# Performance work log

Hardware: AMD Instinct MI355X
Metric: run time of the kernel (lower is better)

The kernel has to match this reference:

```python
import jax, jax.numpy as jnp
import numpy as np


def setup_inputs() -> dict:
    key = jax.random.key(0)
    ks = jax.random.split(key, 5)
    S, B, H = 4096, 32, 512
    scale = 1.0 / np.sqrt(2 * H)
    return {
        "hidden": jax.random.normal(ks[0], (B, H), dtype=jnp.float32),
        "encoder_outputs": jax.random.normal(ks[1], (S, B, H), dtype=jnp.float32),
        "attn_W": jax.random.normal(ks[2], (H, 2 * H), dtype=jnp.float32) * scale,
        "attn_b": jax.random.normal(ks[3], (H,), dtype=jnp.float32) * scale,
        "v_W": jax.random.normal(ks[4], (1, H), dtype=jnp.float32) * (1.0 / np.sqrt(H)),
    }


def reference(hidden, encoder_outputs, attn_W, attn_b, v_W):
    # hidden: [B,H], encoder_outputs: [S,B,H]
    # energy = tanh(concat(hidden_rep, enc) @ attn_W.T + attn_b)
    # Split attn_W into the hidden-part and encoder-part to avoid
    # materializing the repeated/concatenated [S,B,2H] tensor.
    H = hidden.shape[-1]
    Wh, We = attn_W[:, :H], attn_W[:, H:]  # each [H, H]
    # hidden contribution is identical for all seq positions: [B,H]
    h_proj = jnp.einsum('bh,oh->bo', hidden, Wh) + attn_b
    e_proj = jnp.einsum('sbh,oh->sbo', encoder_outputs, We)
    energy = jnp.tanh(h_proj[None, :, :] + e_proj)          # [S,B,H]
    scores = jnp.einsum('sbh,h->sb', energy, v_W[0])        # [S,B]
    attn_weights = jax.nn.softmax(scores.T, axis=1)         # [B,S]
    # context = sum_s w[b,s] * enc[s,b,:]
    context = jnp.einsum('bs,sbh->bh', attn_weights, encoder_outputs)
    return (context, attn_weights)
```

## Files before the change

### kernel.cpp

```cpp
#include <hip/hip_runtime.h>
#include <hip/hip_bf16.h>
#include <math.h>

#define S 4096
#define B 32
#define H 512
#define NSC 16

typedef float f32x16 __attribute__((ext_vector_type(16)));
typedef short s16x8 __attribute__((ext_vector_type(8)));

__device__ __forceinline__ unsigned short f2bf(float x) {
  return __builtin_bit_cast(unsigned short, __float2bfloat16(x));
}
__device__ __forceinline__ float bf2f(unsigned short h) {
  return __builtin_bit_cast(float, ((unsigned)h) << 16);
}
__device__ __forceinline__ float tanh_fast(float x) {
  float e = __expf(2.0f * x);
  return 1.0f - 2.0f / (e + 1.0f);
}

#define GLOAD_LDS16(g, l) __builtin_amdgcn_global_load_lds( \
    (const __attribute__((address_space(1))) void*)(g),     \
    (__attribute__((address_space(3))) void*)(l), 16, 0, 0)

__global__ __launch_bounds__(256) void k_wfrag(const float* __restrict__ W,
                                               unsigned short* __restrict__ WH,
                                               unsigned short* __restrict__ WL) {
  int id = blockIdx.x * 256 + threadIdx.x;
  int lane = id & 63, ks = (id >> 6) & 31, n = id >> 11;
  int o = n * 32 + (lane & 31);
  int kb = ks * 16 + (lane >> 5) * 8;
  const float* src = W + (size_t)o * (2 * H) + H + kb;
  s16x8 h, l;
#pragma unroll
  for (int j = 0; j < 8; ++j) {
    float x = src[j];
    unsigned short hb = f2bf(x);
    h[j] = (short)hb;
    l[j] = (short)f2bf(x - bf2f(hb));
  }
  *(s16x8*)(WH + (size_t)id * 8) = h;
  *(s16x8*)(WL + (size_t)id * 8) = l;
}

__global__ __launch_bounds__(256) void k_hproj(const float* __restrict__ hidden,
                                               const float* __restrict__ W,
                                               const float* __restrict__ bias,
                                               float* __restrict__ hprojT) {
  int blk = blockIdx.x;
  int b = blk >> 3, oc = blk & 7;
  int t = threadIdx.x;
  int o = oc * 64 + (t >> 2);
  int kq = t & 3;
  const float* hrow = hidden + b * H + kq * 128;
  const float* wrow = W + (size_t)o * (2 * H) + kq * 128;
  float p = 0.f;
#pragma unroll 4
  for (int k = 0; k < 128; ++k) p = fmaf(hrow[k], wrow[k], p);
  p += __shfl_xor(p, 1);
  p += __shfl_xor(p, 2);
  if (kq == 0) hprojT[o * B + b] = p + bias[o];
}

#define MFMA32(a, b, c) __builtin_amdgcn_mfma_f32_32x32x16_bf16(a, b, c, 0, 0, 0)

#define STAGE(dstbuf, ph)                                          \
  {                                                                \
    const char* gh_ = WHb + (size_t)(ph) * 16384;                  \
    const char* gl_ = WLb + (size_t)(ph) * 16384;                  \
    _Pragma("unroll")                                              \
    for (int i_ = 0; i_ < 4; ++i_) {                               \
      int co_ = (w * 4 + i_) * 1024;                               \
      GLOAD_LDS16(gh_ + co_ + lane * 16, dstbuf + co_);            \
      GLOAD_LDS16(gl_ + co_ + lane * 16, dstbuf + 16384 + co_);    \
    }                                                              \
  }

__global__ __launch_bounds__(256, 1) void k_scores(const float* __restrict__ enc,
                                                   const char* __restrict__ WHb,
                                                   const char* __restrict__ WLb,
                                                   const float* __restrict__ hprojT,
                                                   const float* __restrict__ vW,
                                                   float* __restrict__ scores) {
  __shared__ char Bb0[32768];
  __shared__ char Bb1[32768];
  int t = threadIdx.x;
  int w = t >> 6, lane = t & 63;
  int wbase = blockIdx.x * 128 + w * 32;
  int arow = wbase + (lane & 31);
  int half = lane >> 5;

  STAGE(Bb0, 0);

  s16x8 ah[32], al[32];
  {
    const float* ap = enc + (size_t)arow * H + half * 8;
#pragma unroll
    for (int ks = 0; ks < 32; ++ks) {
      float4 x0 = *(const float4*)(ap + ks * 16);
      float4 x1 = *(const float4*)(ap + ks * 16 + 4);
      float xs[8] = {x0.x, x0.y, x0.z, x0.w, x1.x, x1.y, x1.z, x1.w};
      s16x8 h, l;
#pragma unroll
      for (int j = 0; j < 8; ++j) {
        unsigned short hb = f2bf(xs[j]);
        h[j] = (short)hb;
        l[j] = (short)f2bf(xs[j] - bf2f(hb));
      }
      ah[ks] = h;
      al[ks] = l;
    }
  }

  float pr[16];
#pragma unroll
  for (int r = 0; r < 16; ++r) pr[r] = 0.f;

  __syncthreads();

  for (int n = 0; n < 16; ++n) {
    f32x16 chh = {}, chl = {}, clh = {};
    STAGE(Bb1, 2 * n + 1);
#pragma unroll
    for (int ks = 0; ks < 16; ++ks) {
      s16x8 b0 = *(const s16x8*)(Bb0 + ks * 1024 + lane * 16);
      s16x8 b1 = *(const s16x8*)(Bb0 + 16384 + ks * 1024 + lane * 16);
      chh = MFMA32(ah[ks], b0, chh);
      chl = MFMA32(ah[ks], b1, chl);
      clh = MFMA32(al[ks], b0, clh);
    }
    __syncthreads();
    if (n < 15) STAGE(Bb0, 2 * n + 2);
#pragma unroll
    for (int ks = 0; ks < 16; ++ks) {
      s16x8 b0 = *(const s16x8*)(Bb1 + ks * 1024 + lane * 16);
      s16x8 b1 = *(const s16x8*)(Bb1 + 16384 + ks * 1024 + lane * 16);
      chh = MFMA32(ah[16 + ks], b0, chh);
      chl = MFMA32(ah[16 + ks], b1, chl);
      clh = MFMA32(al[16 + ks], b0, clh);
    }
    {
      int o = n * 32 + (lane & 31);
      float vw = vW[o];
      const float4* hp4 = (const float4*)(hprojT + o * B + half * 4);
      float4 h0 = hp4[0], h1 = hp4[2], h2 = hp4[4], h3 = hp4[6];
      float hr[16] = {h0.x, h0.y, h0.z, h0.w, h1.x, h1.y, h1.z, h1.w,
                      h2.x, h2.y, h2.z, h2.w, h3.x, h3.y, h3.z, h3.w};
#pragma unroll
      for (int r = 0; r < 16; ++r) {
        float e = (chh[r] + chl[r]) + clh[r] + hr[r];
        pr[r] += vw * tanh_fast(e);
      }
    }
    __syncthreads();
  }

#pragma unroll
  for (int off = 1; off < 32; off <<= 1) {
#pragma unroll
    for (int r = 0; r < 16; ++r) pr[r] += __shfl_xor(pr[r], off);
  }
  if ((lane & 31) == 0) {
    int srow = wbase >> 5;
#pragma unroll
    for (int r = 0; r < 16; ++r) {
      int m = (r & 3) + 8 * (r >> 2) + 4 * half;
      scores[(size_t)m * S + srow] = pr[r];
    }
  }
}

__global__ __launch_bounds__(256) void k_softmax(const float* __restrict__ scores,
                                                 float* __restrict__ outw) {
  int b = blockIdx.x, t = threadIdx.x;
  const float* row = scores + (size_t)b * S;
  float* wrow = outw + (size_t)b * S;
  float m = -1e30f;
  for (int s = t; s < S; s += 256) m = fmaxf(m, row[s]);
#pragma unroll
  for (int off = 32; off; off >>= 1) m = fmaxf(m, __shfl_xor(m, off));
  __shared__ float red[4];
  __shared__ float red2[4];
  int wv = t >> 6, ln = t & 63;
  if (ln == 0) red[wv] = m;
  __syncthreads();
  m = fmaxf(fmaxf(red[0], red[1]), fmaxf(red[2], red[3]));
  float sum = 0.f;
  for (int s = t; s < S; s += 256) {
    float e = __expf(row[s] - m);
    wrow[s] = e;
    sum += e;
  }
#pragma unroll
  for (int off = 32; off; off >>= 1) sum += __shfl_xor(sum, off);
  if (ln == 0) red2[wv] = sum;
  __syncthreads();
  sum = red2[0] + red2[1] + red2[2] + red2[3];
  float inv = 1.f / sum;
  for (int s = t; s < S; s += 256) wrow[s] *= inv;
}

__global__ __launch_bounds__(256) void k_ctxpart(const float* __restrict__ enc,
                                                 const float* __restrict__ w,
                                                 float* __restrict__ part) {
  int b = blockIdx.x, sc = blockIdx.y, t = threadIdx.x;
  const float* wrow = w + (size_t)b * S + sc * (S / NSC);
  float2 acc = {0.f, 0.f};
  for (int ss = 0; ss < S / NSC; ss += 2) {
    int s = sc * (S / NSC) + ss;
    float w0 = wrow[ss], w1 = wrow[ss + 1];
    float2 e0 = ((const float2*)(enc + ((size_t)s * B + b) * H))[t];
    float2 e1 = ((const float2*)(enc + ((size_t)(s + 1) * B + b) * H))[t];
    acc.x = fmaf(w0, e0.x, acc.x);
    acc.y = fmaf(w0, e0.y, acc.y);
    acc.x = fmaf(w1, e1.x, acc.x);
    acc.y = fmaf(w1, e1.y, acc.y);
  }
  ((float2*)(part + ((size_t)b * NSC + sc) * H))[t] = acc;
}

__global__ __launch_bounds__(256) void k_ctxsum(const float* __restrict__ part,
                                                float* __restrict__ ctx) {
  int idx = blockIdx.x * 256 + threadIdx.x;
  int b = idx >> 9, h = idx & 511;
  float sum = 0.f;
#pragma unroll
  for (int sc = 0; sc < NSC; ++sc) sum += part[((size_t)b * NSC + sc) * H + h];
  ctx[idx] = sum;
}

extern "C" void kernel_launch(void* const* d_in, const int* in_sizes, int n_in,
                              void* d_out, int out_size, void* d_ws, size_t ws_size,
                              hipStream_t stream) {
  const float* hidden = (const float*)d_in[0];
  const float* enc    = (const float*)d_in[1];
  const float* W      = (const float*)d_in[2];
  const float* bias   = (const float*)d_in[3];
  const float* vW     = (const float*)d_in[4];

  float* out   = (float*)d_out;
  float* ctx   = out;
  float* attnw = out + B * H;

  float* ws      = (float*)d_ws;
  float* hprojT  = ws;
  float* scores  = ws + B * H;
  float* region = scores + (size_t)B * S;
  unsigned short* WH = (unsigned short*)region;
  unsigned short* WL = (unsigned short*)(region + 131072);
  float* part = region;

  k_wfrag<<<128, 256, 0, stream>>>(W, WH, WL);
  k_hproj<<<256, 256, 0, stream>>>(hidden, W, bias, hprojT);
  k_scores<<<(S * B) / 128, 256, 0, stream>>>(enc, (const char*)WH, (const char*)WL,
                                              hprojT, vW, scores);
  k_softmax<<<B, 256, 0, stream>>>(scores, attnw);
  k_ctxpart<<<dim3(B, NSC), 256, 0, stream>>>(enc, attnw, part);
  k_ctxsum<<<(B * H) / 256, 256, 0, stream>>>(part, ctx);
}
```

Measured before the change: 674.1 us.

## Replace double-buffered weight staging with 4-slot ring and fine-grained waitcnt barriers

Weight staging in the scores kernel moves from two 32KB buffers with full __syncthreads to a four-slot ring of 16KB slices. Each slice is loaded three steps ahead and synchronised with explicit s_waitcnt vmcnt plus s_barrier. The per-n hproj and vW loads are hoisted before the MFMA work so their latency is hidden. The aim is deeper prefetch and fewer full-drain barriers, at the cost of more barriers per iteration and a fragile hand-tuned vmcnt count.

```diff
diff --git a/kernel.cpp b/kernel.cpp
--- a/kernel.cpp
+++ b/kernel.cpp
@@ -66,17 +66,35 @@
 
 #define MFMA32(a, b, c) __builtin_amdgcn_mfma_f32_32x32x16_bf16(a, b, c, 0, 0, 0)
 
-#define STAGE(dstbuf, ph)                                          \
-  {                                                                \
-    const char* gh_ = WHb + (size_t)(ph) * 16384;                  \
-    const char* gl_ = WLb + (size_t)(ph) * 16384;                  \
-    _Pragma("unroll")                                              \
-    for (int i_ = 0; i_ < 4; ++i_) {                               \
-      int co_ = (w * 4 + i_) * 1024;                               \
-      GLOAD_LDS16(gh_ + co_ + lane * 16, dstbuf + co_);            \
-      GLOAD_LDS16(gl_ + co_ + lane * 16, dstbuf + 16384 + co_);    \
-    }                                                              \
-  }
+#define SSTAGE(q)                                                        \
+  {                                                                      \
+    int q_ = (q);                                                        \
+    char* rb_ = Bb + (q_ & 3) * 16384;                                   \
+    const char* gh_ = WHb + (size_t)q_ * 8192 + w * 2048;                \
+    const char* gl_ = WLb + (size_t)q_ * 8192 + w * 2048;                \
+    GLOAD_LDS16(gh_ + lane * 16, rb_ + w * 2048);                        \
+    GLOAD_LDS16(gh_ + 1024 + lane * 16, rb_ + w * 2048 + 1024);          \
+    GLOAD_LDS16(gl_ + lane * 16, rb_ + 8192 + w * 2048);                 \
+    GLOAD_LDS16(gl_ + 1024 + lane * 16, rb_ + 8192 + w * 2048 + 1024);   \
+  }
+
+#define COMPUTE8(q, SUB)                                                 \
+  {                                                                      \
+    const char* rb_ = Bb + ((q) & 3) * 16384 + lane * 16;                \
+    _Pragma("unroll")                                                    \
+    for (int kl_ = 0; kl_ < 8; ++kl_) {                                  \
+      s16x8 b0_ = *(const s16x8*)(rb_ + kl_ * 1024);                     \
+      s16x8 b1_ = *(const s16x8*)(rb_ + 8192 + kl_ * 1024);              \
+      chh = MFMA32(ah[(SUB) * 8 + kl_], b0_, chh);                       \
+      chl = MFMA32(ah[(SUB) * 8 + kl_], b1_, chl);                       \
+      clh = MFMA32(al[(SUB) * 8 + kl_], b0_, clh);                       \
+    }                                                                    \
+  }
+
+#define PIPE_SYNC(N)                                                     \
+  asm volatile("s_waitcnt vmcnt(" #N ")" ::: "memory");                  \
+  __builtin_amdgcn_s_barrier();                                          \
+  __builtin_amdgcn_sched_barrier(0);
 
 __global__ __launch_bounds__(256, 1) void k_scores(const float* __restrict__ enc,
                                                    const char* __restrict__ WHb,
@@ -84,15 +102,15 @@
                                                    const float* __restrict__ hprojT,
                                                    const float* __restrict__ vW,
                                                    float* __restrict__ scores) {
-  __shared__ char Bb0[32768];
-  __shared__ char Bb1[32768];
+  __shared__ char Bb[4 * 16384];
   int t = threadIdx.x;
   int w = t >> 6, lane = t & 63;
   int wbase = blockIdx.x * 128 + w * 32;
   int arow = wbase + (lane & 31);
   int half = lane >> 5;
 
-  STAGE(Bb0, 0);
+  SSTAGE(0);
+  SSTAGE(1);
 
   s16x8 ah[32], al[32];
   {
@@ -114,38 +132,27 @@
     }
   }
 
+  SSTAGE(2);
+
   float pr[16];
 #pragma unroll
   for (int r = 0; r < 16; ++r) pr[r] = 0.f;
 
-  __syncthreads();
-
-  for (int n = 0; n < 16; ++n) {
+  __builtin_amdgcn_s_barrier();
+  __builtin_amdgcn_sched_barrier(0);
+
+  for (int n = 0; n < 15; ++n) {
+    int o = n * 32 + (lane & 31);
+    float vw = vW[o];
+    const float4* hp4 = (const float4*)(hprojT + o * B + half * 4);
+    float4 h0 = hp4[0], h1 = hp4[2], h2 = hp4[4], h3 = hp4[6];
     f32x16 chh = {}, chl = {}, clh = {};
-    STAGE(Bb1, 2 * n + 1);
-#pragma unroll
-    for (int ks = 0; ks < 16; ++ks) {
-      s16x8 b0 = *(const s16x8*)(Bb0 + ks * 1024 + lane * 16);
-      s16x8 b1 = *(const s16x8*)(Bb0 + 16384 + ks * 1024 + lane * 16);
-      chh = MFMA32(ah[ks], b0, chh);
-      chl = MFMA32(ah[ks], b1, chl);
-      clh = MFMA32(al[ks], b0, clh);
-    }
-    __syncthreads();
-    if (n < 15) STAGE(Bb0, 2 * n + 2);
-#pragma unroll
-    for (int ks = 0; ks < 16; ++ks) {
-      s16x8 b0 = *(const s16x8*)(Bb1 + ks * 1024 + lane * 16);
-      s16x8 b1 = *(const s16x8*)(Bb1 + 16384 + ks * 1024 + lane * 16);
-      chh = MFMA32(ah[16 + ks], b0, chh);
-      chl = MFMA32(ah[16 + ks], b1, chl);
-      clh = MFMA32(al[16 + ks], b0, clh);
-    }
+    int q = 4 * n;
+    SSTAGE(q + 3); COMPUTE8(q + 0, 0); PIPE_SYNC(8)
+    SSTAGE(q + 4); COMPUTE8(q + 1, 1); PIPE_SYNC(8)
+    SSTAGE(q + 5); COMPUTE8(q + 2, 2); PIPE_SYNC(8)
+    SSTAGE(q + 6); COMPUTE8(q + 3, 3);
     {
-      int o = n * 32 + (lane & 31);
-      float vw = vW[o];
-      const float4* hp4 = (const float4*)(hprojT + o * B + half * 4);
-      float4 h0 = hp4[0], h1 = hp4[2], h2 = hp4[4], h3 = hp4[6];
       float hr[16] = {h0.x, h0.y, h0.z, h0.w, h1.x, h1.y, h1.z, h1.w,
                       h2.x, h2.y, h2.z, h2.w, h3.x, h3.y, h3.z, h3.w};
 #pragma unroll
@@ -154,7 +161,28 @@
         pr[r] += vw * tanh_fast(e);
       }
     }
-    __syncthreads();
+    PIPE_SYNC(8)
+  }
+
+  {
+    int o = 15 * 32 + (lane & 31);
+    float vw = vW[o];
+    const float4* hp4 = (const float4*)(hprojT + o * B + half * 4);
+    float4 h0 = hp4[0], h1 = hp4[2], h2 = hp4[4], h3 = hp4[6];
+    f32x16 chh = {}, chl = {}, clh = {};
+    SSTAGE(63);    COMPUTE8(60, 0); PIPE_SYNC(8)
+    COMPUTE8(61, 1); PIPE_SYNC(8)
+    COMPUTE8(62, 2); PIPE_SYNC(0)
+    COMPUTE8(63, 3);
+    {
+      float hr[16] = {h0.x, h0.y, h0.z, h0.w, h1.x, h1.y, h1.z, h1.w,
+                      h2.x, h2.y, h2.z, h2.w, h3.x, h3.y, h3.z, h3.w};
+#pragma unroll
+      for (int r = 0; r < 16; ++r) {
+        float e = (chh[r] + chl[r]) + clh[r] + hr[r];
+        pr[r] += vw * tanh_fast(e);
+      }
+    }
   }
 
 #pragma unroll
```

Measured after the change: 641.9 us. 4.8% less time.
